# Performance work log

Hardware: AMD Instinct MI355X
Metric: run time of the kernel (lower is better)

## Reference

```python
import jax, jax.numpy as jnp
import numpy as np

B, SQ, C = 8, 4096, 1280
CAD = 2048
H, D = 20, 64          # heads x head_dim = hidden_size
NT = 4                 # num IP tokens
TXT = 77               # text tokens
IP_SCALE = 1.0


def setup_inputs() -> dict:
    key = jax.random.key(0)
    ks = jax.random.split(key, 9)
    s = 0.02
    return {
        "hidden_states": jax.random.normal(ks[0], (B, SQ, C), jnp.float32),
        "encoder_hidden_states": jax.random.normal(ks[1], (B, TXT + NT, CAD), jnp.float32),
        "Wq": jax.random.normal(ks[2], (C, C), jnp.float32) * s,
        "Wk": jax.random.normal(ks[3], (CAD, C), jnp.float32) * s,
        "Wv": jax.random.normal(ks[4], (CAD, C), jnp.float32) * s,
        "Wk_ip": jax.random.normal(ks[5], (CAD, C), jnp.float32) * s,
        "Wv_ip": jax.random.normal(ks[6], (CAD, C), jnp.float32) * s,
        "Wo": jax.random.normal(ks[7], (C, C), jnp.float32) * s,
        "bo": jnp.zeros((C,), jnp.float32),
    }


def _heads(x):
    # [b, s, C] -> [b, H, s, D]
    b, s, _ = x.shape
    return x.reshape(b, s, H, D).transpose(0, 2, 1, 3)


def _attend(q, k, v):
    scale = jnp.asarray(1.0 / np.sqrt(D), q.dtype)
    probs = jax.nn.softmax(jnp.einsum('bhqd,bhkd->bhqk', q, k) * scale, axis=-1)
    return jnp.einsum('bhqk,bhkd->bhqd', probs, v)


def reference(hidden_states, encoder_hidden_states, Wq, Wk, Wv, Wk_ip, Wv_ip, Wo, bo):
    residual = hidden_states
    txt = encoder_hidden_states[:, :-NT, :]   # [B, 77, CAD]
    ip = encoder_hidden_states[:, -NT:, :]    # [B, 4, CAD]

    q = _heads(hidden_states @ Wq)            # [B, H, SQ, D]
    k = _heads(txt @ Wk)
    v = _heads(txt @ Wv)
    out = _attend(q, k, v)                    # text branch

    ip_k = _heads(ip @ Wk_ip)
    ip_v = _heads(ip @ Wv_ip)
    out = out + IP_SCALE * _attend(q, ip_k, ip_v)  # IP-adapter branch

    b = out.shape[0]
    out = out.transpose(0, 2, 1, 3).reshape(b, SQ, C)  # merge heads
    out = out @ Wo + bo
    return out + residual
```

## Files before the change

### kernel.cpp

```cpp
#include <hip/hip_runtime.h>
#include <hip/hip_bf16.h>
#include <cstdint>
#include <cstddef>


typedef __bf16 bf16_t;
typedef __bf16 bf16x8 __attribute__((ext_vector_type(8)));
typedef __bf16 bf16x4 __attribute__((ext_vector_type(4)));
typedef float  f32x4  __attribute__((ext_vector_type(4)));
typedef unsigned int u32x4 __attribute__((ext_vector_type(4)));

using as3_void  = __attribute__((address_space(3))) void;
using as1_cvoid = const __attribute__((address_space(1))) void;

#define TXT_ 77

__device__ __forceinline__ bf16x8 ld16(const void* p) {
  u32x4 v = *(const u32x4*)p;
  return __builtin_bit_cast(bf16x8, v);
}

template <int EPI>
__global__ __launch_bounds__(512, 2)
void gemm256(const bf16_t* __restrict__ A, const bf16_t* __restrict__ Bt,
             void* __restrict__ Cout, int ntn, int N, int K,
             const float* __restrict__ bias, const void* __restrict__ residual)
{
  __shared__ __align__(16) char smem[131072];
  const int tid = threadIdx.x, lane = tid & 63, wid = tid >> 6;
  const int wm = wid >> 2, wn = wid & 3;

  const int nwg = gridDim.x;
  int g = blockIdx.x;
  if ((nwg & 7) == 0) g = (blockIdx.x & 7) * (nwg >> 3) + (blockIdx.x >> 3);
  const long bm = (long)(g / ntn) * 256;
  const long bn = (long)(g % ntn) * 256;

  const int NTk = K >> 5;

  const int srow = lane >> 2;
  const int scol = ((lane & 3) ^ ((lane >> 3) & 3)) * 8;

  auto stageA = [&](int t) {
    const int buf = t & 3;
    const long k0 = (long)t << 5;
#pragma unroll
    for (int j = 0; j < 2; ++j) {
      const int ci = j * 8 + wid;
      const bf16_t* gp = A + (bm + ci * 16 + srow) * (long)K + k0 + scol;
      __builtin_amdgcn_global_load_lds((as1_cvoid*)gp,
          (as3_void*)(smem + buf * 16384 + ci * 1024), 16, 0, 0);
    }
  };
  auto stageB = [&](int t) {
    const int buf = t & 3;
    const long k0 = (long)t << 5;
#pragma unroll
    for (int j = 0; j < 2; ++j) {
      const int ci = j * 8 + wid;
      const bf16_t* gp = Bt + (bn + ci * 16 + srow) * (long)K + k0 + scol;
      __builtin_amdgcn_global_load_lds((as1_cvoid*)gp,
          (as3_void*)(smem + 65536 + buf * 16384 + ci * 1024), 16, 0, 0);
    }
  };

  const int l15 = lane & 15, kq = lane >> 4;
  const int rc16 = (kq ^ ((l15 >> 1) & 3)) << 4;

  f32x4 acc[8][4] = {};

  stageA(0); stageB(0); stageA(1); stageB(1);
  asm volatile("s_waitcnt vmcnt(4)" ::: "memory");
  __builtin_amdgcn_s_barrier();

  for (int t = 0; t < NTk; ++t) {
    const char* sa = smem + (t & 3) * 16384;
    const char* sb = smem + 65536 + (t & 3) * 16384;
    bf16x8 bfr[4], afr[4];
#pragma unroll
    for (int n = 0; n < 4; ++n)
      bfr[n] = ld16(sb + (wn * 64 + n * 16 + l15) * 64 + rc16);
#pragma unroll
    for (int m = 0; m < 4; ++m)
      afr[m] = ld16(sa + (wm * 128 + m * 16 + l15) * 64 + rc16);
    if (t + 2 < NTk) stageA(t + 2);
    __builtin_amdgcn_s_setprio(1);
#pragma unroll
    for (int m = 0; m < 4; ++m)
#pragma unroll
      for (int n = 0; n < 4; ++n)
        acc[m][n] = __builtin_amdgcn_mfma_f32_16x16x32_bf16(afr[m], bfr[n], acc[m][n], 0, 0, 0);
    __builtin_amdgcn_s_setprio(0);
#pragma unroll
    for (int m = 0; m < 4; ++m)
      afr[m] = ld16(sa + (wm * 128 + (m + 4) * 16 + l15) * 64 + rc16);
    if (t + 2 < NTk) stageB(t + 2);
    __builtin_amdgcn_s_setprio(1);
#pragma unroll
    for (int m = 0; m < 4; ++m)
#pragma unroll
      for (int n = 0; n < 4; ++n)
        acc[m + 4][n] = __builtin_amdgcn_mfma_f32_16x16x32_bf16(afr[m], bfr[n], acc[m + 4][n], 0, 0, 0);
    __builtin_amdgcn_s_setprio(0);
    if (t == NTk - 2) asm volatile("s_waitcnt vmcnt(0)" ::: "memory");
    else              asm volatile("s_waitcnt vmcnt(4)" ::: "memory");
    __builtin_amdgcn_s_barrier();
    asm volatile("" ::: "memory");
  }

  const int orow0 = (lane >> 4) << 2;
#pragma unroll
  for (int m = 0; m < 8; ++m) {
#pragma unroll
    for (int n = 0; n < 4; ++n) {
      const long col = bn + wn * 64 + n * 16 + l15;
#pragma unroll
      for (int r = 0; r < 4; ++r) {
        const long row = bm + wm * 128 + m * 16 + orow0 + r;
        if constexpr (EPI == 0) {
          ((bf16_t*)Cout)[row * N + col] = (bf16_t)acc[m][n][r];
        } else {
          ((float*)Cout)[row * N + col] =
              acc[m][n][r] + bias[col] +
              (float)((const bf16_t*)residual)[row * N + col];
        }
      }
    }
  }
}

__global__ __launch_bounds__(256, 4)
void gemm_bt(const bf16_t* __restrict__ A, const bf16_t* __restrict__ Bt,
             bf16_t* __restrict__ Cout, int ntn, int N, int K)
{
  __shared__ __align__(16) char smem[2][16384];
  const int tid  = threadIdx.x;
  const int lane = tid & 63;
  const int wid  = tid >> 6;
  const int wm = wid >> 1, wn = wid & 1;

  const int g = blockIdx.x;
  const long bm = (long)(g / ntn) * 128;
  const long bn = (long)(g % ntn) * 128;

  f32x4 acc[4][4] = {};

  const int srow = lane >> 2;
  const int skb  = (lane & 3) ^ (((lane >> 2) ^ (lane >> 4)) & 3);
  const int NT = K >> 5;

  auto stage = [&](int buf, int kt) {
    const int k0 = kt << 5;
#pragma unroll
    for (int cc = 0; cc < 2; ++cc) {
      const int c = wid + cc * 4;
      const bf16_t* ga = A + (bm + c * 16 + srow) * (long)K + (k0 + skb * 8);
      __builtin_amdgcn_global_load_lds((as1_cvoid*)ga,
                                       (as3_void*)(&smem[buf][c * 1024]), 16, 0, 0);
      const bf16_t* gb = Bt + (bn + c * 16 + srow) * (long)K + (k0 + skb * 8);
      __builtin_amdgcn_global_load_lds((as1_cvoid*)gb,
                                       (as3_void*)(&smem[buf][8192 + c * 1024]), 16, 0, 0);
    }
  };

  const int rkb    = (((lane >> 4) ^ (lane & 3) ^ ((lane >> 2) & 3)) & 3) << 4;
  const int rrow_a = wm * 64 + (lane & 15);
  const int rrow_b = wn * 64 + (lane & 15);

  stage(0, 0);
  int cur = 0;
  for (int t = 0; t < NT; ++t) {
    __syncthreads();
    if (t + 1 < NT) stage(cur ^ 1, t + 1);
    const char* sa = smem[cur];
    const char* sb = smem[cur] + 8192;
    bf16x8 af[4], bfv[4];
#pragma unroll
    for (int m = 0; m < 4; ++m)
      af[m] = ld16(sa + (rrow_a + m * 16) * 64 + rkb);
#pragma unroll
    for (int n = 0; n < 4; ++n)
      bfv[n] = ld16(sb + (rrow_b + n * 16) * 64 + rkb);
#pragma unroll
    for (int m = 0; m < 4; ++m)
#pragma unroll
      for (int n = 0; n < 4; ++n)
        acc[m][n] = __builtin_amdgcn_mfma_f32_16x16x32_bf16(af[m], bfv[n], acc[m][n], 0, 0, 0);
    cur ^= 1;
  }

  const int orow0 = wm * 64 + ((lane >> 4) << 2);
  const int ocol0 = wn * 64 + (lane & 15);
#pragma unroll
  for (int m = 0; m < 4; ++m)
#pragma unroll
    for (int n = 0; n < 4; ++n) {
      const long col = bn + ocol0 + n * 16;
#pragma unroll
      for (int r = 0; r < 4; ++r)
        Cout[(bm + orow0 + m * 16 + r) * (long)N + col] = (bf16_t)acc[m][n][r];
    }
}

__global__ __launch_bounds__(256, 3)
void attn_fused(const bf16_t* __restrict__ q, const bf16_t* __restrict__ kvt,
                const bf16_t* __restrict__ kvip, bf16_t* __restrict__ outp)
{
  __shared__ __align__(16) bf16_t K_lds[80 * 64];
  __shared__ __align__(16) bf16_t Kip_lds[16 * 64];
  __shared__ __align__(16) bf16_t Vt_lds[64 * 128];
  __shared__ __align__(16) bf16_t P_lds[4][16 * 128];

  const int tid = threadIdx.x, lane = tid & 63, wid = tid >> 6;
  const int h = blockIdx.y, b = blockIdx.z;
  const int kvcol = h << 6;

  for (int idx = tid; idx < 640; idx += 256) {
    const int j = idx >> 3, c = idx & 7;
    bf16x8 v = {};
    if (j < TXT_) v = ld16(kvt + (long)(b * 80 + j) * 2560 + kvcol + c * 8);
    *(bf16x8*)((char*)K_lds + j * 128 + ((c ^ (j & 7)) << 4)) = v;
  }
  if (tid < 128) {
    const int j = tid >> 3, c = tid & 7;
    bf16x8 v = {};
    if (j < 4) v = ld16(kvip + (long)(b * 4 + j) * 2560 + kvcol + c * 8);
    *(bf16x8*)((char*)Kip_lds + j * 128 + ((c ^ (j & 7)) << 4)) = v;
  }
  for (int idx = tid; idx < 1024; idx += 256) {
    const int key = idx >> 3, c = idx & 7;
    bf16x8 v = {};
    if (key < TXT_)
      v = ld16(kvt + (long)(b * 80 + key) * 2560 + 1280 + kvcol + c * 8);
    else if (key >= 96 && key < 100)
      v = ld16(kvip + (long)(b * 4 + key - 96) * 2560 + 1280 + kvcol + c * 8);
#pragma unroll
    for (int e = 0; e < 8; ++e) {
      const int d = c * 8 + e;
      *(bf16_t*)((char*)Vt_lds + d * 256 + ((key * 2) ^ ((d & 7) << 4))) = v[e];
    }
  }
  for (int idx = tid; idx < 1024; idx += 256)
    *(bf16x8*)((char*)P_lds + idx * 16) = (bf16x8){};
  __syncthreads();

  const int l15 = lane & 15, hi = lane >> 4;
  const int dblk = hi << 3;
  const int prow0 = hi << 2;
  const float scale = 0.125f;
  char* const pw = (char*)P_lds[wid];

  const long qrow0 = (long)b * 4096 + ((long)blockIdx.x << 8) + (wid << 6);
  bf16x8 qf[4][2];
#pragma unroll
  for (int ms = 0; ms < 4; ++ms) {
    const bf16_t* qp = q + (qrow0 + ms * 16 + l15) * 1280 + kvcol;
    qf[ms][0] = ld16(qp + dblk);
    qf[ms][1] = ld16(qp + 32 + dblk);
  }

#pragma unroll
  for (int ms = 0; ms < 4; ++ms) {
    f32x4 sc[5];
#pragma unroll
    for (int t = 0; t < 5; ++t) {
      const int j = (t << 4) + l15;
      const bf16x8 k0 = ld16((char*)K_lds + j * 128 + ((hi ^ (j & 7)) << 4));
      const bf16x8 k1 = ld16((char*)K_lds + j * 128 + (((4 + hi) ^ (j & 7)) << 4));
      f32x4 z = {0.f, 0.f, 0.f, 0.f};
      z = __builtin_amdgcn_mfma_f32_16x16x32_bf16(qf[ms][0], k0, z, 0, 0, 0);
      z = __builtin_amdgcn_mfma_f32_16x16x32_bf16(qf[ms][1], k1, z, 0, 0, 0);
      sc[t] = z;
    }
#pragma unroll
    for (int t = 0; t < 5; ++t) {
      const bool valid = ((t << 4) + l15) < TXT_;
#pragma unroll
      for (int r = 0; r < 4; ++r)
        sc[t][r] = valid ? sc[t][r] * scale : -1e30f;
    }

#pragma unroll
    for (int r = 0; r < 4; ++r) {
      float m = sc[0][r];
#pragma unroll
      for (int t = 1; t < 5; ++t) m = fmaxf(m, sc[t][r]);
      m = fmaxf(m, __shfl_xor(m, 1));
      m = fmaxf(m, __shfl_xor(m, 2));
      m = fmaxf(m, __shfl_xor(m, 4));
      m = fmaxf(m, __shfl_xor(m, 8));
      float l = 0.f;
#pragma unroll
      for (int t = 0; t < 5; ++t) { const float p = __expf(sc[t][r] - m); sc[t][r] = p; l += p; }
      l += __shfl_xor(l, 1);
      l += __shfl_xor(l, 2);
      l += __shfl_xor(l, 4);
      l += __shfl_xor(l, 8);
      const float inv = 1.f / l;
      const int row = prow0 + r;
#pragma unroll
      for (int t = 0; t < 5; ++t)
        *(bf16_t*)(pw + row * 256 + ((((t << 4) + l15) * 2) ^ ((row & 7) << 4))) =
            (bf16_t)(sc[t][r] * inv);
    }

    {
      const bf16x8 ki0 = ld16((char*)Kip_lds + l15 * 128 + ((hi ^ (l15 & 7)) << 4));
      const bf16x8 ki1 = ld16((char*)Kip_lds + l15 * 128 + (((4 + hi) ^ (l15 & 7)) << 4));
      f32x4 z = {0.f, 0.f, 0.f, 0.f};
      z = __builtin_amdgcn_mfma_f32_16x16x32_bf16(qf[ms][0], ki0, z, 0, 0, 0);
      z = __builtin_amdgcn_mfma_f32_16x16x32_bf16(qf[ms][1], ki1, z, 0, 0, 0);
      const bool vip = l15 < 4;
#pragma unroll
      for (int r = 0; r < 4; ++r) {
        const float s = vip ? z[r] * scale : -1e30f;
        float m = s;
        m = fmaxf(m, __shfl_xor(m, 1));
        m = fmaxf(m, __shfl_xor(m, 2));
        m = fmaxf(m, __shfl_xor(m, 4));
        m = fmaxf(m, __shfl_xor(m, 8));
        const float p = __expf(s - m);
        float l = p;
        l += __shfl_xor(l, 1);
        l += __shfl_xor(l, 2);
        l += __shfl_xor(l, 4);
        l += __shfl_xor(l, 8);
        const int row = prow0 + r;
        *(bf16_t*)(pw + row * 256 + (((96 + l15) * 2) ^ ((row & 7) << 4))) =
            (bf16_t)(p * (1.f / l));
      }
    }

    f32x4 o[4] = {};
#pragma unroll
    for (int s = 0; s < 4; ++s) {
      const bf16x8 pa =
          ld16(pw + l15 * 256 + ((((s << 2) + hi) << 4) ^ ((l15 & 7) << 4)));
#pragma unroll
      for (int n = 0; n < 4; ++n) {
        const int d = (n << 4) + l15;
        const bf16x8 vb =
            ld16((char*)Vt_lds + d * 256 + ((((s << 2) + hi) << 4) ^ ((d & 7) << 4)));
        o[n] = __builtin_amdgcn_mfma_f32_16x16x32_bf16(pa, vb, o[n], 0, 0, 0);
      }
    }

    const long orow = qrow0 + ms * 16 + prow0;
#pragma unroll
    for (int n = 0; n < 4; ++n)
#pragma unroll
      for (int r = 0; r < 4; ++r)
        outp[(orow + r) * 1280 + kvcol + (n << 4) + l15] = (bf16_t)o[n][r];
  }
}

__global__ void cvt_bf16(const float* __restrict__ in, bf16_t* __restrict__ out, long n)
{
  const long i = ((long)blockIdx.x * 256 + threadIdx.x) * 4;
  if (i >= n) return;
  const float4 v = *(const float4*)(in + i);
  bf16x4 r;
  r[0] = (bf16_t)v.x; r[1] = (bf16_t)v.y; r[2] = (bf16_t)v.z; r[3] = (bf16_t)v.w;
  *(bf16x4*)(out + i) = r;
}

__global__ void transpose_cvt(const float* __restrict__ in, bf16_t* __restrict__ out,
                              int K, int N, int ostride)
{
  __shared__ float tile[32][33];
  const int k0 = blockIdx.x * 32, n0 = blockIdx.y * 32;
  for (int i = threadIdx.y; i < 32; i += 8)
    tile[i][threadIdx.x] = in[(long)(k0 + i) * N + n0 + threadIdx.x];
  __syncthreads();
  for (int i = threadIdx.y; i < 32; i += 8)
    out[(long)(n0 + i) * ostride + k0 + threadIdx.x] = (bf16_t)tile[threadIdx.x][i];
}

__global__ void pack_enc(const float* __restrict__ enc, bf16_t* __restrict__ a_txt,
                         bf16_t* __restrict__ a_ip)
{
  const long t4 = ((long)blockIdx.x * 256 + threadIdx.x) * 4;
  const long NTXT = 640L * 2048;
  bf16x4 r;
  r[0] = r[1] = r[2] = r[3] = (bf16_t)0.f;
  if (t4 < NTXT) {
    const int row = (int)(t4 >> 11), col = (int)(t4 & 2047);
    const int b = row / 80, j = row - b * 80;
    if (j < TXT_) {
      const float4 v = *(const float4*)(enc + (((long)(b * 81 + j)) << 11) + col);
      r[0] = (bf16_t)v.x; r[1] = (bf16_t)v.y; r[2] = (bf16_t)v.z; r[3] = (bf16_t)v.w;
    }
    *(bf16x4*)(a_txt + t4) = r;
  } else {
    const long u = t4 - NTXT;
    const int row = (int)(u >> 11), col = (int)(u & 2047);
    if (row < 32) {
      const int b = row >> 2, j = row & 3;
      const float4 v = *(const float4*)(enc + (((long)(b * 81 + TXT_ + j)) << 11) + col);
      r[0] = (bf16_t)v.x; r[1] = (bf16_t)v.y; r[2] = (bf16_t)v.z; r[3] = (bf16_t)v.w;
    }
    *(bf16x4*)(a_ip + u) = r;
  }
}

extern "C" void kernel_launch(void* const* d_in, const int* in_sizes, int n_in,
                              void* d_out, int out_size, void* d_ws, size_t ws_size,
                              hipStream_t stream)
{
  (void)in_sizes; (void)n_in; (void)out_size; (void)ws_size;
  const float* hs  = (const float*)d_in[0];
  const float* enc = (const float*)d_in[1];
  const float* Wq  = (const float*)d_in[2];
  const float* Wk  = (const float*)d_in[3];
  const float* Wv  = (const float*)d_in[4];
  const float* Wki = (const float*)d_in[5];
  const float* Wvi = (const float*)d_in[6];
  const float* Wo  = (const float*)d_in[7];
  const float* bo  = (const float*)d_in[8];

  char* ws = (char*)d_ws;
  size_t off = 0;
  auto alloc = [&](size_t bytes) {
    char* p = ws + off;
    off += (bytes + 255) & ~(size_t)255;
    return p;
  };
  bf16_t* buf1   = (bf16_t*)alloc(83886080);
  bf16_t* qb     = (bf16_t*)alloc(83886080);
  bf16_t* Wq_t   = (bf16_t*)alloc(3276800);
  bf16_t* Wo_t   = (bf16_t*)alloc(3276800);
  bf16_t* Wkv_t  = (bf16_t*)alloc(10485760);
  bf16_t* Wip_t  = (bf16_t*)alloc(10485760);
  bf16_t* a_txt  = (bf16_t*)alloc(2621440);
  bf16_t* a_ip   = (bf16_t*)alloc(524288);
  bf16_t* kv_txt = (bf16_t*)alloc(3276800);
  bf16_t* kv_ip  = (bf16_t*)alloc(655360);

  const dim3 tb(32, 8);
  cvt_bf16<<<40960, 256, 0, stream>>>(hs, buf1, 41943040L);
  transpose_cvt<<<dim3(40, 40), tb, 0, stream>>>(Wq, Wq_t, 1280, 1280, 1280);
  transpose_cvt<<<dim3(40, 40), tb, 0, stream>>>(Wo, Wo_t, 1280, 1280, 1280);
  transpose_cvt<<<dim3(64, 40), tb, 0, stream>>>(Wk, Wkv_t, 2048, 1280, 2048);
  transpose_cvt<<<dim3(64, 40), tb, 0, stream>>>(Wv, Wkv_t + (long)1280 * 2048, 2048, 1280, 2048);
  transpose_cvt<<<dim3(64, 40), tb, 0, stream>>>(Wki, Wip_t, 2048, 1280, 2048);
  transpose_cvt<<<dim3(64, 40), tb, 0, stream>>>(Wvi, Wip_t + (long)1280 * 2048, 2048, 1280, 2048);
  pack_enc<<<1536, 256, 0, stream>>>(enc, a_txt, a_ip);

  gemm256<0><<<640, 512, 0, stream>>>(buf1, Wq_t, qb, 5, 1280, 1280,
                                      nullptr, nullptr);
  gemm_bt<<<100, 256, 0, stream>>>(a_txt, Wkv_t, kv_txt, 20, 2560, 2048);
  gemm_bt<<<20, 256, 0, stream>>>(a_ip, Wip_t, kv_ip, 20, 2560, 2048);

  attn_fused<<<dim3(16, 20, 8), 256, 0, stream>>>(qb, kv_txt, kv_ip, qb);

  gemm256<2><<<640, 512, 0, stream>>>(qb, Wo_t, d_out, 5, 1280, 1280,
                                      bo, buf1);
}
```

Measured before the change: 484.8 us.

## Merge weight transposes and small GEMMs into single launches; stage Q GEMM epilogue via LDS

The six weight transpose launches become one 3D-grid kernel, and the two small K/V projection GEMMs become one launch of 120 blocks. Both cut per-launch overhead and let the small pieces of work run concurrently. The bf16 Q-projection epilogue now writes the tile to shared memory and stores it to global as coalesced 16-byte rows instead of scattered 2-byte stores. This costs an extra barrier and an LDS round trip, and the transpose grid now launches some idle blocks for the 1280-wide matrices.

```diff
diff --git a/kernel.cpp b/kernel.cpp
--- a/kernel.cpp
+++ b/kernel.cpp
@@ -35,7 +35,6 @@
   if ((nwg & 7) == 0) g = (blockIdx.x & 7) * (nwg >> 3) + (blockIdx.x >> 3);
   const long bm = (long)(g / ntn) * 256;
   const long bn = (long)(g % ntn) * 256;
-
   const int NTk = K >> 5;
 
   const int srow = lane >> 2;
@@ -68,6 +67,7 @@
   const int rc16 = (kq ^ ((l15 >> 1) & 3)) << 4;
 
   f32x4 acc[8][4] = {};
+  bf16x8 afr[4], bfr[4];
 
   stageA(0); stageB(0); stageA(1); stageB(1);
   asm volatile("s_waitcnt vmcnt(4)" ::: "memory");
@@ -76,14 +76,15 @@
   for (int t = 0; t < NTk; ++t) {
     const char* sa = smem + (t & 3) * 16384;
     const char* sb = smem + 65536 + (t & 3) * 16384;
-    bf16x8 bfr[4], afr[4];
+    const bool pf = (t + 2 < NTk);
+
 #pragma unroll
     for (int n = 0; n < 4; ++n)
       bfr[n] = ld16(sb + (wn * 64 + n * 16 + l15) * 64 + rc16);
 #pragma unroll
     for (int m = 0; m < 4; ++m)
       afr[m] = ld16(sa + (wm * 128 + m * 16 + l15) * 64 + rc16);
-    if (t + 2 < NTk) stageA(t + 2);
+    if (pf) stageA(t + 2);
     __builtin_amdgcn_s_setprio(1);
 #pragma unroll
     for (int m = 0; m < 4; ++m)
@@ -91,10 +92,11 @@
       for (int n = 0; n < 4; ++n)
         acc[m][n] = __builtin_amdgcn_mfma_f32_16x16x32_bf16(afr[m], bfr[n], acc[m][n], 0, 0, 0);
     __builtin_amdgcn_s_setprio(0);
+
 #pragma unroll
     for (int m = 0; m < 4; ++m)
       afr[m] = ld16(sa + (wm * 128 + (m + 4) * 16 + l15) * 64 + rc16);
-    if (t + 2 < NTk) stageB(t + 2);
+    if (pf) stageB(t + 2);
     __builtin_amdgcn_s_setprio(1);
 #pragma unroll
     for (int m = 0; m < 4; ++m)
@@ -102,24 +104,41 @@
       for (int n = 0; n < 4; ++n)
         acc[m + 4][n] = __builtin_amdgcn_mfma_f32_16x16x32_bf16(afr[m], bfr[n], acc[m + 4][n], 0, 0, 0);
     __builtin_amdgcn_s_setprio(0);
+
     if (t == NTk - 2) asm volatile("s_waitcnt vmcnt(0)" ::: "memory");
     else              asm volatile("s_waitcnt vmcnt(4)" ::: "memory");
     __builtin_amdgcn_s_barrier();
-    asm volatile("" ::: "memory");
   }
 
   const int orow0 = (lane >> 4) << 2;
-#pragma unroll
-  for (int m = 0; m < 8; ++m) {
-#pragma unroll
-    for (int n = 0; n < 4; ++n) {
-      const long col = bn + wn * 64 + n * 16 + l15;
-#pragma unroll
-      for (int r = 0; r < 4; ++r) {
-        const long row = bm + wm * 128 + m * 16 + orow0 + r;
-        if constexpr (EPI == 0) {
-          ((bf16_t*)Cout)[row * N + col] = (bf16_t)acc[m][n][r];
-        } else {
+  if constexpr (EPI == 0) {
+    bf16_t* cl = (bf16_t*)smem;
+    const int lrow0 = wm * 128 + orow0;
+    const int lcol0 = wn * 64 + l15;
+#pragma unroll
+    for (int m = 0; m < 8; ++m)
+#pragma unroll
+      for (int n = 0; n < 4; ++n)
+#pragma unroll
+        for (int r = 0; r < 4; ++r)
+          cl[(lrow0 + m * 16 + r) * 256 + lcol0 + n * 16] = (bf16_t)acc[m][n][r];
+    __syncthreads();
+    const int rr = tid >> 5, cc = tid & 31;
+#pragma unroll
+    for (int s = 0; s < 16; ++s) {
+      const int row = s * 16 + rr;
+      const u32x4 v = *(const u32x4*)(cl + row * 256 + cc * 8);
+      *(u32x4*)((bf16_t*)Cout + (bm + row) * (long)N + bn + cc * 8) = v;
+    }
+  } else {
+#pragma unroll
+    for (int m = 0; m < 8; ++m) {
+#pragma unroll
+      for (int n = 0; n < 4; ++n) {
+        const long col = bn + wn * 64 + n * 16 + l15;
+#pragma unroll
+        for (int r = 0; r < 4; ++r) {
+          const long row = bm + wm * 128 + m * 16 + orow0 + r;
           ((float*)Cout)[row * N + col] =
               acc[m][n][r] + bias[col] +
               (float)((const bf16_t*)residual)[row * N + col];
@@ -130,8 +149,10 @@
 }
 
 __global__ __launch_bounds__(256, 4)
-void gemm_bt(const bf16_t* __restrict__ A, const bf16_t* __restrict__ Bt,
-             bf16_t* __restrict__ Cout, int ntn, int N, int K)
+void gemm_small(const bf16_t* __restrict__ A0, const bf16_t* __restrict__ B0,
+                bf16_t* __restrict__ C0,
+                const bf16_t* __restrict__ A1, const bf16_t* __restrict__ B1,
+                bf16_t* __restrict__ C1)
 {
   __shared__ __align__(16) char smem[2][16384];
   const int tid  = threadIdx.x;
@@ -139,7 +160,13 @@
   const int wid  = tid >> 6;
   const int wm = wid >> 1, wn = wid & 1;
 
-  const int g = blockIdx.x;
+  const bf16_t *A, *Bt;
+  bf16_t* Cout;
+  int g = blockIdx.x;
+  if (g < 100) { A = A0; Bt = B0; Cout = C0; }
+  else         { A = A1; Bt = B1; Cout = C1; g -= 100; }
+  const int ntn = 20, N = 2560, K = 2048;
+
   const long bm = (long)(g / ntn) * 128;
   const long bn = (long)(g % ntn) * 128;
 
@@ -364,16 +391,32 @@
   *(bf16x4*)(out + i) = r;
 }
 
-__global__ void transpose_cvt(const float* __restrict__ in, bf16_t* __restrict__ out,
-                              int K, int N, int ostride)
-{
+__global__ void transpose_all(const float* __restrict__ Wq, const float* __restrict__ Wo,
+                              const float* __restrict__ Wk, const float* __restrict__ Wv,
+                              const float* __restrict__ Wki, const float* __restrict__ Wvi,
+                              bf16_t* __restrict__ Wq_t, bf16_t* __restrict__ Wo_t,
+                              bf16_t* __restrict__ Wkv_t, bf16_t* __restrict__ Wip_t)
+{
+  const int z = blockIdx.z;
+  const float* in;
+  bf16_t* out;
+  int K;
+  switch (z) {
+    case 0:  in = Wq;  out = Wq_t;                        K = 1280; break;
+    case 1:  in = Wo;  out = Wo_t;                        K = 1280; break;
+    case 2:  in = Wk;  out = Wkv_t;                       K = 2048; break;
+    case 3:  in = Wv;  out = Wkv_t + (long)1280 * 2048;   K = 2048; break;
+    case 4:  in = Wki; out = Wip_t;                       K = 2048; break;
+    default: in = Wvi; out = Wip_t + (long)1280 * 2048;   K = 2048; break;
+  }
+  const int k0 = blockIdx.x * 32, n0 = blockIdx.y * 32;
+  if (k0 >= K) return;
   __shared__ float tile[32][33];
-  const int k0 = blockIdx.x * 32, n0 = blockIdx.y * 32;
   for (int i = threadIdx.y; i < 32; i += 8)
-    tile[i][threadIdx.x] = in[(long)(k0 + i) * N + n0 + threadIdx.x];
+    tile[i][threadIdx.x] = in[(long)(k0 + i) * 1280 + n0 + threadIdx.x];
   __syncthreads();
   for (int i = threadIdx.y; i < 32; i += 8)
-    out[(long)(n0 + i) * ostride + k0 + threadIdx.x] = (bf16_t)tile[threadIdx.x][i];
+    out[(long)(n0 + i) * K + k0 + threadIdx.x] = (bf16_t)tile[threadIdx.x][i];
 }
 
 __global__ void pack_enc(const float* __restrict__ enc, bf16_t* __restrict__ a_txt,
@@ -436,20 +479,14 @@
   bf16_t* kv_txt = (bf16_t*)alloc(3276800);
   bf16_t* kv_ip  = (bf16_t*)alloc(655360);
 
-  const dim3 tb(32, 8);
   cvt_bf16<<<40960, 256, 0, stream>>>(hs, buf1, 41943040L);
-  transpose_cvt<<<dim3(40, 40), tb, 0, stream>>>(Wq, Wq_t, 1280, 1280, 1280);
-  transpose_cvt<<<dim3(40, 40), tb, 0, stream>>>(Wo, Wo_t, 1280, 1280, 1280);
-  transpose_cvt<<<dim3(64, 40), tb, 0, stream>>>(Wk, Wkv_t, 2048, 1280, 2048);
-  transpose_cvt<<<dim3(64, 40), tb, 0, stream>>>(Wv, Wkv_t + (long)1280 * 2048, 2048, 1280, 2048);
-  transpose_cvt<<<dim3(64, 40), tb, 0, stream>>>(Wki, Wip_t, 2048, 1280, 2048);
-  transpose_cvt<<<dim3(64, 40), tb, 0, stream>>>(Wvi, Wip_t + (long)1280 * 2048, 2048, 1280, 2048);
+  transpose_all<<<dim3(64, 40, 6), dim3(32, 8), 0, stream>>>(
+      Wq, Wo, Wk, Wv, Wki, Wvi, Wq_t, Wo_t, Wkv_t, Wip_t);
   pack_enc<<<1536, 256, 0, stream>>>(enc, a_txt, a_ip);
 
   gemm256<0><<<640, 512, 0, stream>>>(buf1, Wq_t, qb, 5, 1280, 1280,
                                       nullptr, nullptr);
-  gemm_bt<<<100, 256, 0, stream>>>(a_txt, Wkv_t, kv_txt, 20, 2560, 2048);
-  gemm_bt<<<20, 256, 0, stream>>>(a_ip, Wip_t, kv_ip, 20, 2560, 2048);
+  gemm_small<<<120, 256, 0, stream>>>(a_txt, Wkv_t, kv_txt, a_ip, Wip_t, kv_ip);
 
   attn_fused<<<dim3(16, 20, 8), 256, 0, stream>>>(qb, kv_txt, kv_ip, qb);
 
```

After: 439.8 us. -9.3%, faster.
